# Kernel optimization log

Hardware: AMD Instinct MI355X
Metric: run time of the kernel (lower is better)

Reference implementation:

```python
import jax, jax.numpy as jnp
import numpy as np

N_EMBD = 768
N_HEAD = 12
LN_EPS = 1e-5


def _linear_params(key, fan_in, fan_out):
    kw, kb = jax.random.split(key)
    bound = 1.0 / np.sqrt(fan_in)
    W = jax.random.uniform(kw, (fan_in, fan_out), jnp.float32, -bound, bound)
    b = jax.random.uniform(kb, (fan_out,), jnp.float32, -bound, bound)
    return W, b


def setup_inputs() -> dict:
    key = jax.random.key(0)
    ks = jax.random.split(key, 6)
    x = jax.random.normal(ks[0], (8, 1024, N_EMBD), jnp.float32)
    W_attn, b_attn = _linear_params(ks[1], N_EMBD, 3 * N_EMBD)
    W_proj, b_proj = _linear_params(ks[2], N_EMBD, N_EMBD)
    W_fc, b_fc = _linear_params(ks[3], N_EMBD, 4 * N_EMBD)
    W_fc2, b_fc2 = _linear_params(ks[4], 4 * N_EMBD, N_EMBD)
    return {
        "x": x,
        "ln1_g": jnp.ones((N_EMBD,), jnp.float32),
        "ln1_b": jnp.zeros((N_EMBD,), jnp.float32),
        "W_attn": W_attn, "b_attn": b_attn,
        "W_proj": W_proj, "b_proj": b_proj,
        "ln2_g": jnp.ones((N_EMBD,), jnp.float32),
        "ln2_b": jnp.zeros((N_EMBD,), jnp.float32),
        "W_fc": W_fc, "b_fc": b_fc,
        "W_fc2": W_fc2, "b_fc2": b_fc2,
    }


def _layernorm(x, g, b):
    mu = jnp.mean(x, axis=-1, keepdims=True)
    var = jnp.var(x, axis=-1, keepdims=True)
    return (x - mu) * jax.lax.rsqrt(var + LN_EPS) * g + b


def _attn(x, W_attn, b_attn, W_proj, b_proj):
    B, T, C = x.shape
    hd = C // N_HEAD
    qkv = x @ W_attn + b_attn  # [B,T,3C]
    q, k, v = jnp.split(qkv, 3, axis=-1)
    q = q.reshape(B, T, N_HEAD, hd).transpose(0, 2, 1, 3)  # [B,H,T,hd]
    k = k.reshape(B, T, N_HEAD, hd).transpose(0, 2, 1, 3)
    v = v.reshape(B, T, N_HEAD, hd).transpose(0, 2, 1, 3)
    scores = jnp.einsum('bhqd,bhkd->bhqk', q, k) * (1.0 / np.sqrt(hd))
    mask = jnp.tril(jnp.ones((T, T), bool))
    scores = jnp.where(mask, scores, -jnp.inf)
    attn = jax.nn.softmax(scores, axis=-1)
    y = jnp.einsum('bhqk,bhkd->bhqd', attn, v)
    y = y.transpose(0, 2, 1, 3).reshape(B, T, C)
    return y @ W_proj + b_proj


def reference(x, ln1_g, ln1_b, W_attn, b_attn, W_proj, b_proj,
              ln2_g, ln2_b, W_fc, b_fc, W_fc2, b_fc2):
    x = x + _attn(_layernorm(x, ln1_g, ln1_b), W_attn, b_attn, W_proj, b_proj)
    h = _layernorm(x, ln2_g, ln2_b)
    h = jax.nn.gelu(h @ W_fc + b_fc, approximate=False)  # torch GELU default = exact erf
    x = x + h @ W_fc2 + b_fc2
    return x
```

## Files before the change

### kernel.cpp

```cpp
#include <hip/hip_runtime.h>
#include <hip/hip_bf16.h>
#include <stdint.h>

#define DEV __device__ __forceinline__

typedef __attribute__((ext_vector_type(8))) short     short8;
typedef __attribute__((ext_vector_type(4))) float     f32x4;
typedef __attribute__((ext_vector_type(4))) unsigned short ushort4v;

DEV float bf2f(unsigned short u) { return __uint_as_float(((uint32_t)u) << 16); }
DEV unsigned short f2bf(float f) {
    uint32_t x = __float_as_uint(f);
    return (unsigned short)((x + 0x7FFFu + ((x >> 16) & 1u)) >> 16);
}

DEV f32x4 mfma16(short8 a, short8 b, f32x4 c) {
    return __builtin_amdgcn_mfma_f32_16x16x32_bf16(a, b, c, 0, 0, 0);
}

#define AS1C const __attribute__((address_space(1)))
#define AS3  __attribute__((address_space(3)))

DEV void gload_lds16(const void* g, void* l) {
    __builtin_amdgcn_global_load_lds((AS1C void*)g, (AS3 void*)l, 16, 0, 0);
}

__global__ __launch_bounds__(256) void ln_kernel(const float* __restrict__ x,
                                                 const float* __restrict__ g,
                                                 const float* __restrict__ b,
                                                 unsigned short* __restrict__ out)
{
    const int lane = threadIdx.x & 63;
    const int row  = blockIdx.x * 4 + (threadIdx.x >> 6);
    const float* xr = x + (size_t)row * 768;

    f32x4 v[3];
    float s = 0.f, sq = 0.f;
#pragma unroll
    for (int i = 0; i < 3; ++i) {
        v[i] = *(const f32x4*)(xr + i * 256 + lane * 4);
#pragma unroll
        for (int j = 0; j < 4; ++j) { s += v[i][j]; sq = fmaf(v[i][j], v[i][j], sq); }
    }
#pragma unroll
    for (int off = 32; off; off >>= 1) { s += __shfl_xor(s, off); sq += __shfl_xor(sq, off); }
    const float mean = s * (1.0f / 768.0f);
    const float rstd = rsqrtf(sq * (1.0f / 768.0f) - mean * mean + 1e-5f);

#pragma unroll
    for (int i = 0; i < 3; ++i) {
        f32x4 gg = *(const f32x4*)(g + i * 256 + lane * 4);
        f32x4 bb = *(const f32x4*)(b + i * 256 + lane * 4);
        ushort4v o;
#pragma unroll
        for (int j = 0; j < 4; ++j) o[j] = f2bf((v[i][j] - mean) * rstd * gg[j] + bb[j]);
        *(ushort4v*)(out + (size_t)row * 768 + i * 256 + lane * 4) = o;
    }
}

__global__ __launch_bounds__(256) void wconv_kernel(const float* __restrict__ W,
                                                    unsigned short* __restrict__ Wt,
                                                    int K, int N)
{
    __shared__ float t[32][33];
    const int tx = threadIdx.x & 31, ty = threadIdx.x >> 5;
    const int n0 = blockIdx.x * 32, k0 = blockIdx.y * 32;
#pragma unroll
    for (int i = 0; i < 4; ++i)
        t[ty + i * 8][tx] = W[(size_t)(k0 + ty + i * 8) * N + n0 + tx];
    __syncthreads();
#pragma unroll
    for (int i = 0; i < 4; ++i)
        Wt[(size_t)(n0 + ty + i * 8) * K + k0 + tx] = f2bf(t[tx][ty + i * 8]);
}

template <int EPI>
__global__ __launch_bounds__(256) void gemm_bt(const unsigned short* __restrict__ A,
                                               const unsigned short* __restrict__ Bt,
                                               const float* __restrict__ bias,
                                               const float* __restrict__ res,
                                               float* __restrict__ outf,
                                               unsigned short* __restrict__ outh,
                                               int M, int N, int K)
{
    __shared__ unsigned short As[128 * 32];
    __shared__ unsigned short Bs[128 * 32];
    const int tid = threadIdx.x;
    const int lane = tid & 63, wv = tid >> 6;
    const int r16 = lane & 15, g4 = lane >> 4;
    const int wm = wv >> 1, wn = wv & 1;
    const int n0 = blockIdx.x * 128, m0 = blockIdx.y * 128;

    f32x4 acc[4][4] = {};

    for (int k0 = 0; k0 < K; k0 += 32) {
#pragma unroll
        for (int i = 0; i < 2; ++i) {
            const int chunk0 = wv * 128 + i * 64;
            const int c = chunk0 + lane;
            const unsigned short* ga = A  + (size_t)(m0 + (c >> 2)) * K + k0 + (c & 3) * 8;
            const unsigned short* gb = Bt + (size_t)(n0 + (c >> 2)) * K + k0 + (c & 3) * 8;
            gload_lds16(ga, (char*)As + (size_t)chunk0 * 16);
            gload_lds16(gb, (char*)Bs + (size_t)chunk0 * 16);
        }
        __syncthreads();

        short8 af[4], bfr[4];
#pragma unroll
        for (int i = 0; i < 4; ++i)
            af[i] = *(const short8*)(As + (wm * 64 + i * 16 + r16) * 32 + g4 * 8);
#pragma unroll
        for (int j = 0; j < 4; ++j)
            bfr[j] = *(const short8*)(Bs + (wn * 64 + j * 16 + r16) * 32 + g4 * 8);
#pragma unroll
        for (int i = 0; i < 4; ++i)
#pragma unroll
            for (int j = 0; j < 4; ++j)
                acc[i][j] = mfma16(af[i], bfr[j], acc[i][j]);
        __syncthreads();
    }

#pragma unroll
    for (int i = 0; i < 4; ++i) {
#pragma unroll
        for (int j = 0; j < 4; ++j) {
            const int row = m0 + wm * 64 + i * 16 + g4 * 4;
            const int col = n0 + wn * 64 + j * 16 + r16;
            const float bv = bias[col];
#pragma unroll
            for (int r = 0; r < 4; ++r) {
                const float v = acc[i][j][r] + bv;
                const size_t idx = (size_t)(row + r) * N + col;
                if constexpr (EPI == 0) {
                    outh[idx] = f2bf(v);
                } else if constexpr (EPI == 1) {
                    outf[idx] = v + res[idx];
                } else {
                    const float ge = 0.5f * v * (1.0f + erff(v * 0.70710678118654752f));
                    outh[idx] = f2bf(ge);
                }
            }
        }
    }
}

__global__ __launch_bounds__(256) void attn_kernel(const unsigned short* __restrict__ qkv,
                                                   unsigned short* __restrict__ out)
{
    __shared__ alignas(16) unsigned short K_lds[2][64][64];
    __shared__ alignas(16) unsigned short Vt[64][64];
    __shared__ alignas(16) unsigned short P_lds[4][2][16][72];

    const int tid  = threadIdx.x;
    const int lane = tid & 63, w = tid >> 6;
    const int r16 = lane & 15, g4 = lane >> 4;
    const int qb = blockIdx.x, h = blockIdx.y, b = blockIdx.z;
    const int C3 = 2304, T = 1024;
    const int qt  = qb * 4 + w;
    const int gr0 = b * T + qt * 32;
    const int qc  = h * 64;
    const int ns  = 2 * qb + 2;

    const unsigned short* kbase = qkv + (size_t)(b * T) * C3 + 768 + qc;
    const unsigned short* vbase = kbase + 768;

    short8 qf[2][2];
#pragma unroll
    for (int mt = 0; mt < 2; ++mt)
#pragma unroll
        for (int ks = 0; ks < 2; ++ks) {
            short8 v = *(const short8*)(qkv + (size_t)(gr0 + mt * 16 + r16) * C3 + qc + ks * 32 + g4 * 8);
#pragma unroll
            for (int j = 0; j < 8; ++j)
                v[j] = (short)f2bf(bf2f((unsigned short)v[j]) * 0.125f);
            qf[mt][ks] = v;
        }

    auto STAGE_K = [&](int st, int buf) {
#pragma unroll
        for (int i = 0; i < 2; ++i) {
            const int cb = i * 256 + w * 64;
            const int c  = cb + lane;
            const int row = c >> 3, k2 = c & 7;
            gload_lds16(kbase + (size_t)(st * 64 + row) * C3 + (size_t)((k2 ^ (row & 7)) * 8),
                        (char*)K_lds[buf] + (size_t)cb * 16);
        }
    };

    f32x4 o[2][4] = {};
    float mst[2][4], lst[2][4];
#pragma unroll
    for (int mt = 0; mt < 2; ++mt)
#pragma unroll
        for (int r = 0; r < 4; ++r) { mst[mt][r] = -1e30f; lst[mt][r] = 0.f; }

    short8 vreg[2];
    STAGE_K(0, 0);
#pragma unroll
    for (int i = 0; i < 2; ++i)
        vreg[i] = *(const short8*)(vbase + (size_t)lane * C3 + w * 16 + i * 8);

    for (int s = 0; s < ns; ++s) {
        __syncthreads();
#pragma unroll
        for (int i = 0; i < 2; ++i)
#pragma unroll
            for (int j = 0; j < 8; ++j)
                Vt[w * 16 + i * 8 + j][(((lane >> 3) ^ j) << 3) | (lane & 7)] =
                    (unsigned short)vreg[i][j];
        __syncthreads();

        if (s + 1 < ns) {
            STAGE_K(s + 1, (s + 1) & 1);
#pragma unroll
            for (int i = 0; i < 2; ++i)
                vreg[i] = *(const short8*)(vbase + (size_t)((s + 1) * 64 + lane) * C3 + w * 16 + i * 8);
        }

        if (s * 64 <= qt * 32 + 31) {
            const int buf = s & 1;
            short8 kf[4][2];
#pragma unroll
            for (int kt = 0; kt < 4; ++kt)
#pragma unroll
                for (int ks = 0; ks < 2; ++ks) {
                    const int row = kt * 16 + r16;
                    const int pc  = (ks * 4 + g4) ^ (row & 7);
                    kf[kt][ks] = *(const short8*)&K_lds[buf][row][pc * 8];
                }
            f32x4 sv[2][4] = {};
#pragma unroll
            for (int mt = 0; mt < 2; ++mt)
#pragma unroll
                for (int kt = 0; kt < 4; ++kt)
#pragma unroll
                    for (int ks = 0; ks < 2; ++ks)
                        sv[mt][kt] = mfma16(qf[mt][ks], kf[kt][ks], sv[mt][kt]);

            if (s * 64 + 63 > qt * 32) {
#pragma unroll
                for (int mt = 0; mt < 2; ++mt)
#pragma unroll
                    for (int kt = 0; kt < 4; ++kt)
#pragma unroll
                        for (int r = 0; r < 4; ++r)
                            if (s * 64 + kt * 16 + r16 > qt * 32 + mt * 16 + g4 * 4 + r)
                                sv[mt][kt][r] = -1e30f;
            }

#pragma unroll
            for (int mt = 0; mt < 2; ++mt) {
#pragma unroll
                for (int r = 0; r < 4; ++r) {
                    float mx = fmaxf(fmaxf(sv[mt][0][r], sv[mt][1][r]),
                                     fmaxf(sv[mt][2][r], sv[mt][3][r]));
#pragma unroll
                    for (int off = 8; off; off >>= 1) mx = fmaxf(mx, __shfl_xor(mx, off));
                    const float mnew  = fmaxf(mst[mt][r], mx);
                    const float alpha = __expf(mst[mt][r] - mnew);
                    mst[mt][r] = mnew;
                    float p[4], rs = 0.f;
#pragma unroll
                    for (int kt = 0; kt < 4; ++kt) {
                        p[kt] = __expf(sv[mt][kt][r] - mnew);
                        rs += p[kt];
                    }
#pragma unroll
                    for (int off = 8; off; off >>= 1) rs += __shfl_xor(rs, off);
                    lst[mt][r] = lst[mt][r] * alpha + rs;
#pragma unroll
                    for (int kt = 0; kt < 4; ++kt)
                        P_lds[w][mt][g4 * 4 + r][kt * 16 + r16] = f2bf(p[kt]);
#pragma unroll
                    for (int n = 0; n < 4; ++n) o[mt][n][r] *= alpha;
                }
            }

            short8 pa[2][2];
#pragma unroll
            for (int mt = 0; mt < 2; ++mt)
#pragma unroll
                for (int h2 = 0; h2 < 2; ++h2)
                    pa[mt][h2] = *(const short8*)&P_lds[w][mt][r16][h2 * 32 + g4 * 8];
            short8 vf2[2][4];
#pragma unroll
            for (int h2 = 0; h2 < 2; ++h2)
#pragma unroll
                for (int n = 0; n < 4; ++n)
                    vf2[h2][n] = *(const short8*)&Vt[n * 16 + r16][((h2 * 4 + g4) ^ (r16 & 7)) << 3];
#pragma unroll
            for (int h2 = 0; h2 < 2; ++h2)
#pragma unroll
                for (int n = 0; n < 4; ++n) {
                    o[0][n] = mfma16(pa[0][h2], vf2[h2][n], o[0][n]);
                    o[1][n] = mfma16(pa[1][h2], vf2[h2][n], o[1][n]);
                }
        }
    }

#pragma unroll
    for (int mt = 0; mt < 2; ++mt)
#pragma unroll
        for (int n = 0; n < 4; ++n)
#pragma unroll
            for (int r = 0; r < 4; ++r)
                out[(size_t)(gr0 + mt * 16 + g4 * 4 + r) * 768 + qc + n * 16 + r16] =
                    f2bf(o[mt][n][r] / lst[mt][r]);
}

extern "C" void kernel_launch(void* const* d_in, const int* in_sizes, int n_in,
                              void* d_out, int out_size, void* d_ws, size_t ws_size,
                              hipStream_t stream)
{
    const float* x     = (const float*)d_in[0];
    const float* ln1g  = (const float*)d_in[1];
    const float* ln1b  = (const float*)d_in[2];
    const float* Wattn = (const float*)d_in[3];
    const float* battn = (const float*)d_in[4];
    const float* Wproj = (const float*)d_in[5];
    const float* bproj = (const float*)d_in[6];
    const float* ln2g  = (const float*)d_in[7];
    const float* ln2b  = (const float*)d_in[8];
    const float* Wfc   = (const float*)d_in[9];
    const float* bfc   = (const float*)d_in[10];
    const float* Wfc2  = (const float*)d_in[11];
    const float* bfc2  = (const float*)d_in[12];
    float* out = (float*)d_out;

    char* p = (char*)d_ws;
    auto alloc = [&](size_t bytes) { char* q = p; p += (bytes + 255) & ~(size_t)255; return q; };
    unsigned short* wt_attn = (unsigned short*)alloc(768ull * 2304 * 2);
    unsigned short* wt_proj = (unsigned short*)alloc(768ull * 768 * 2);
    unsigned short* wt_fc   = (unsigned short*)alloc(768ull * 3072 * 2);
    unsigned short* wt_fc2  = (unsigned short*)alloc(3072ull * 768 * 2);
    unsigned short* bufA    = (unsigned short*)alloc(8192ull * 768 * 2);
    unsigned short* bufB    = (unsigned short*)alloc(8192ull * 3072 * 2);
    float*          x1      = (float*)alloc(8192ull * 768 * 4);

    const int M = 8192;

    wconv_kernel<<<dim3(2304 / 32, 768 / 32), 256, 0, stream>>>(Wattn, wt_attn, 768, 2304);
    wconv_kernel<<<dim3(768 / 32, 768 / 32), 256, 0, stream>>>(Wproj, wt_proj, 768, 768);
    wconv_kernel<<<dim3(3072 / 32, 768 / 32), 256, 0, stream>>>(Wfc, wt_fc, 768, 3072);
    wconv_kernel<<<dim3(768 / 32, 3072 / 32), 256, 0, stream>>>(Wfc2, wt_fc2, 3072, 768);

    ln_kernel<<<2048, 256, 0, stream>>>(x, ln1g, ln1b, bufA);

    gemm_bt<0><<<dim3(2304 / 128, M / 128), 256, 0, stream>>>(
        bufA, wt_attn, battn, (const float*)nullptr, (float*)nullptr, bufB, M, 2304, 768);

    attn_kernel<<<dim3(8, 12, 8), 256, 0, stream>>>(bufB, bufA);

    gemm_bt<1><<<dim3(768 / 128, M / 128), 256, 0, stream>>>(
        bufA, wt_proj, bproj, x, x1, (unsigned short*)nullptr, M, 768, 768);

    ln_kernel<<<2048, 256, 0, stream>>>(x1, ln2g, ln2b, bufA);

    gemm_bt<2><<<dim3(3072 / 128, M / 128), 256, 0, stream>>>(
        bufA, wt_fc, bfc, (const float*)nullptr, (float*)nullptr, bufB, M, 3072, 768);

    gemm_bt<1><<<dim3(768 / 128, M / 128), 256, 0, stream>>>(
        bufB, wt_fc2, bfc2, x1, out, (unsigned short*)nullptr, M, 768, 3072);
}
```

Before: 468.5 us.

## Add 64-row residual GEMM, double-buffer attention V tile, reorder attention blocks

Adds a new gemm_bt64 kernel with 64x128 tiles for the two N=768 residual GEMMs. This doubles the block count (768 vs 384) so the GPU's compute units are better filled. The attention kernel now double-buffers the transposed V tile, which removes one barrier per iteration, and uses manual waitcnt/s_barrier. It also linearizes the grid so the heaviest causal query blocks launch first. The new GEMM has no double buffering and uses an unswizzled LDS layout, so it risks bank conflicts and exposed load latency.

```diff
diff --git a/kernel.cpp b/kernel.cpp
--- a/kernel.cpp
+++ b/kernel.cpp
@@ -144,17 +144,79 @@
     }
 }
 
+__global__ __launch_bounds__(256) void gemm_bt64(const unsigned short* __restrict__ A,
+                                                 const unsigned short* __restrict__ Bt,
+                                                 const float* __restrict__ bias,
+                                                 const float* __restrict__ res,
+                                                 float* __restrict__ outf,
+                                                 int M, int N, int K)
+{
+    __shared__ unsigned short As[64 * 32];
+    __shared__ unsigned short Bs[128 * 32];
+    const int tid = threadIdx.x;
+    const int lane = tid & 63, wv = tid >> 6;
+    const int r16 = lane & 15, g4 = lane >> 4;
+    const int m0 = blockIdx.x * 64, n0 = blockIdx.y * 128;
+
+    f32x4 acc[4][2] = {};
+
+    for (int k0 = 0; k0 < K; k0 += 32) {
+        const int cb = wv * 64;
+        const int c  = cb + lane;
+        gload_lds16(A + (size_t)(m0 + (c >> 2)) * K + k0 + (c & 3) * 8,
+                    (char*)As + (size_t)cb * 16);
+        gload_lds16(Bt + (size_t)(n0 + (c >> 2)) * K + k0 + (c & 3) * 8,
+                    (char*)Bs + (size_t)cb * 16);
+        gload_lds16(Bt + (size_t)(n0 + ((c + 256) >> 2)) * K + k0 + (c & 3) * 8,
+                    (char*)Bs + (size_t)(cb + 256) * 16);
+        __syncthreads();
+
+        short8 af[4], bfr[2];
+#pragma unroll
+        for (int i = 0; i < 4; ++i)
+            af[i] = *(const short8*)(As + (i * 16 + r16) * 32 + g4 * 8);
+#pragma unroll
+        for (int j = 0; j < 2; ++j)
+            bfr[j] = *(const short8*)(Bs + (wv * 32 + j * 16 + r16) * 32 + g4 * 8);
+#pragma unroll
+        for (int i = 0; i < 4; ++i)
+#pragma unroll
+            for (int j = 0; j < 2; ++j)
+                acc[i][j] = mfma16(af[i], bfr[j], acc[i][j]);
+        __syncthreads();
+    }
+
+#pragma unroll
+    for (int i = 0; i < 4; ++i) {
+#pragma unroll
+        for (int j = 0; j < 2; ++j) {
+            const int row = m0 + i * 16 + g4 * 4;
+            const int col = n0 + wv * 32 + j * 16 + r16;
+            const float bv = bias[col];
+#pragma unroll
+            for (int r = 0; r < 4; ++r) {
+                const size_t idx = (size_t)(row + r) * N + col;
+                outf[idx] = acc[i][j][r] + bv + res[idx];
+            }
+        }
+    }
+}
+
 __global__ __launch_bounds__(256) void attn_kernel(const unsigned short* __restrict__ qkv,
                                                    unsigned short* __restrict__ out)
 {
     __shared__ alignas(16) unsigned short K_lds[2][64][64];
-    __shared__ alignas(16) unsigned short Vt[64][64];
+    __shared__ alignas(16) unsigned short Vt[2][64][64];
     __shared__ alignas(16) unsigned short P_lds[4][2][16][72];
 
     const int tid  = threadIdx.x;
     const int lane = tid & 63, w = tid >> 6;
     const int r16 = lane & 15, g4 = lane >> 4;
-    const int qb = blockIdx.x, h = blockIdx.y, b = blockIdx.z;
+    const int bid = blockIdx.x;
+    const int qb  = 7 - (bid / 96);
+    const int rem = bid % 96;
+    const int h   = rem % 12;
+    const int b   = rem / 12;
     const int C3 = 2304, T = 1024;
     const int qt  = qb * 4 + w;
     const int gr0 = b * T + qt * 32;
@@ -186,6 +248,13 @@
                         (char*)K_lds[buf] + (size_t)cb * 16);
         }
     };
+    auto WRITE_VT = [&](int buf, short8 v0, short8 v1) {
+#pragma unroll
+        for (int j = 0; j < 8; ++j) {
+            Vt[buf][w * 16 + j]     [((((lane >> 3) ^ j) << 3) | (lane & 7))] = (unsigned short)v0[j];
+            Vt[buf][w * 16 + 8 + j] [((((lane >> 3) ^ j) << 3) | (lane & 7))] = (unsigned short)v1[j];
+        }
+    };
 
     f32x4 o[2][4] = {};
     float mst[2][4], lst[2][4];
@@ -194,27 +263,25 @@
 #pragma unroll
         for (int r = 0; r < 4; ++r) { mst[mt][r] = -1e30f; lst[mt][r] = 0.f; }
 
-    short8 vreg[2];
     STAGE_K(0, 0);
-#pragma unroll
-    for (int i = 0; i < 2; ++i)
-        vreg[i] = *(const short8*)(vbase + (size_t)lane * C3 + w * 16 + i * 8);
+    {
+        short8 v0 = *(const short8*)(vbase + (size_t)lane * C3 + w * 16);
+        short8 v1 = *(const short8*)(vbase + (size_t)lane * C3 + w * 16 + 8);
+        asm volatile("s_waitcnt vmcnt(0)" ::: "memory");
+        WRITE_VT(0, v0, v1);
+    }
 
     for (int s = 0; s < ns; ++s) {
-        __syncthreads();
-#pragma unroll
-        for (int i = 0; i < 2; ++i)
-#pragma unroll
-            for (int j = 0; j < 8; ++j)
-                Vt[w * 16 + i * 8 + j][(((lane >> 3) ^ j) << 3) | (lane & 7)] =
-                    (unsigned short)vreg[i][j];
-        __syncthreads();
-
-        if (s + 1 < ns) {
+        asm volatile("s_waitcnt lgkmcnt(0)" ::: "memory");
+        asm volatile("s_barrier" ::: "memory");
+        __builtin_amdgcn_sched_barrier(0);
+
+        short8 vb0, vb1;
+        const bool more = (s + 1 < ns);
+        if (more) {
             STAGE_K(s + 1, (s + 1) & 1);
-#pragma unroll
-            for (int i = 0; i < 2; ++i)
-                vreg[i] = *(const short8*)(vbase + (size_t)((s + 1) * 64 + lane) * C3 + w * 16 + i * 8);
+            vb0 = *(const short8*)(vbase + (size_t)((s + 1) * 64 + lane) * C3 + w * 16);
+            vb1 = *(const short8*)(vbase + (size_t)((s + 1) * 64 + lane) * C3 + w * 16 + 8);
         }
 
         if (s * 64 <= qt * 32 + 31) {
@@ -287,7 +354,7 @@
             for (int h2 = 0; h2 < 2; ++h2)
 #pragma unroll
                 for (int n = 0; n < 4; ++n)
-                    vf2[h2][n] = *(const short8*)&Vt[n * 16 + r16][((h2 * 4 + g4) ^ (r16 & 7)) << 3];
+                    vf2[h2][n] = *(const short8*)&Vt[buf][n * 16 + r16][((h2 * 4 + g4) ^ (r16 & 7)) << 3];
 #pragma unroll
             for (int h2 = 0; h2 < 2; ++h2)
 #pragma unroll
@@ -295,6 +362,11 @@
                     o[0][n] = mfma16(pa[0][h2], vf2[h2][n], o[0][n]);
                     o[1][n] = mfma16(pa[1][h2], vf2[h2][n], o[1][n]);
                 }
+        }
+
+        if (more) {
+            asm volatile("s_waitcnt vmcnt(0)" ::: "memory");
+            WRITE_VT((s + 1) & 1, vb0, vb1);
         }
     }
 
@@ -349,16 +421,16 @@
     gemm_bt<0><<<dim3(2304 / 128, M / 128), 256, 0, stream>>>(
         bufA, wt_attn, battn, (const float*)nullptr, (float*)nullptr, bufB, M, 2304, 768);
 
-    attn_kernel<<<dim3(8, 12, 8), 256, 0, stream>>>(bufB, bufA);
-
-    gemm_bt<1><<<dim3(768 / 128, M / 128), 256, 0, stream>>>(
-        bufA, wt_proj, bproj, x, x1, (unsigned short*)nullptr, M, 768, 768);
+    attn_kernel<<<dim3(768), 256, 0, stream>>>(bufB, bufA);
+
+    gemm_bt64<<<dim3(M / 64, 768 / 128), 256, 0, stream>>>(
+        bufA, wt_proj, bproj, x, x1, M, 768, 768);
 
     ln_kernel<<<2048, 256, 0, stream>>>(x1, ln2g, ln2b, bufA);
 
     gemm_bt<2><<<dim3(3072 / 128, M / 128), 256, 0, stream>>>(
         bufA, wt_fc, bfc, (const float*)nullptr, (float*)nullptr, bufB, M, 3072, 768);
 
-    gemm_bt<1><<<dim3(768 / 128, M / 128), 256, 0, stream>>>(
-        bufB, wt_fc2, bfc2, x1, out, (unsigned short*)nullptr, M, 768, 3072);
-}
+    gemm_bt64<<<dim3(M / 64, 768 / 128), 256, 0, stream>>>(
+        bufB, wt_fc2, bfc2, x1, out, M, 768, 3072);
+}
```

After: 396.1 us. -15.5%, faster.
